# Performance work log

Measured on AMD Instinct MI355X. Metric: run time of the kernel, lower is better.

Reference implementation:

```python
import jax, jax.numpy as jnp
import numpy as np

N_NODES = 50000
N_EDGES = 800000
N_GRAPHS = 64
HEADS = 8
HID = 16
D = HEADS * HID  # 128
N_CLASSES = 10
NEG_SLOPE = 0.2
N_LAYERS = 5


def setup_inputs() -> dict:
    key = jax.random.key(0)
    ks = jax.random.split(key, 12)
    x = jax.random.normal(ks[0], (N_NODES, D), dtype=jnp.float32)
    edge_index = jax.random.randint(ks[1], (2, N_EDGES), 0, N_NODES, dtype=jnp.int32)
    batch = jnp.sort(jax.random.randint(ks[2], (N_NODES,), 0, N_GRAPHS, dtype=jnp.int32))
    s = 1.0 / np.sqrt(D)
    # all 5 GATv2 layers share the same shapes (in = 8*hidden = 128); stack on axis 0
    Wl = jax.random.normal(ks[3], (N_LAYERS, D, D), dtype=jnp.float32) * s
    bl = jnp.zeros((N_LAYERS, D), dtype=jnp.float32)
    Wr = jax.random.normal(ks[4], (N_LAYERS, D, D), dtype=jnp.float32) * s
    br = jnp.zeros((N_LAYERS, D), dtype=jnp.float32)
    att = jax.random.normal(ks[5], (N_LAYERS, HEADS, HID), dtype=jnp.float32) * (1.0 / np.sqrt(HID))
    bias = jnp.zeros((N_LAYERS, D), dtype=jnp.float32)
    Wout = jax.random.normal(ks[6], (D, N_CLASSES), dtype=jnp.float32) * s
    bout = jnp.zeros((N_CLASSES,), dtype=jnp.float32)
    return {"x": x, "edge_index": edge_index, "batch": batch,
            "Wl": Wl, "bl": bl, "Wr": Wr, "br": br, "att": att, "bias": bias,
            "Wout": Wout, "bout": bout}


def gatv2_layer(x, src, dst, Wl, bl, Wr, br, att, bias):
    # x: [N, D_in]; returns [N, HEADS*HID]
    n = x.shape[0]
    xl = (x @ Wl + bl).reshape(n, HEADS, HID)   # source/message transform
    xr = (x @ Wr + br).reshape(n, HEADS, HID)   # target transform
    # GATv2 attention: att . leaky_relu(xl_j + xr_i) per edge, per head
    e = jax.nn.leaky_relu(xl[src] + xr[dst], NEG_SLOPE)          # [E, H, C]
    logits = jnp.einsum('ehc,hc->eh', e, att)                    # [E, H]
    # segment-softmax over incoming edges of each dst node
    m = jax.ops.segment_max(logits, dst, num_segments=n)         # [N, H]
    p = jnp.exp(logits - m[dst])
    denom = jax.ops.segment_sum(p, dst, num_segments=n)          # [N, H]
    alpha = p / denom[dst]                                       # [E, H]
    msg = xl[src] * alpha[:, :, None]                            # [E, H, C]
    out = jax.ops.segment_sum(msg, dst, num_segments=n)
    return out.reshape(n, HEADS * HID) + bias


def reference(x, edge_index, batch, Wl, bl, Wr, br, att, bias, Wout, bout):
    n = x.shape[0]
    # GATv2Conv(add_self_loops=True): append self loops to the edge list
    loops = jnp.arange(n, dtype=edge_index.dtype)
    src = jnp.concatenate([edge_index[0], loops])
    dst = jnp.concatenate([edge_index[1], loops])
    h = x
    for l in range(N_LAYERS):
        h = gatv2_layer(h, src, dst, Wl[l], bl[l], Wr[l], br[l], att[l], bias[l])
        h = jax.nn.elu(h)
    # global mean pool over graphs
    sums = jax.ops.segment_sum(h, batch, num_segments=N_GRAPHS)       # [G, D]
    counts = jax.ops.segment_sum(jnp.ones((n,), h.dtype), batch, num_segments=N_GRAPHS)
    pooled = sums / jnp.maximum(counts, 1.0)[:, None]
    logits = pooled @ Wout + bout
    return jax.nn.log_softmax(logits, axis=1)
```

## Files before the change

kernel.cpp:

```cpp
#include <hip/hip_runtime.h>
#include <hip/hip_bf16.h>
#include <math.h>

#define DD 128
#define HEADS 8
#define HID 16
#define NEG_SLOPE 0.2f
#define N_LAYERS 5
#define N_GRAPHS 64
#define N_CLASSES 10

typedef __bf16 bf16x8 __attribute__((ext_vector_type(8)));
typedef float f32x4 __attribute__((ext_vector_type(4)));

__device__ __forceinline__ float bflo(unsigned u) { return __uint_as_float(u << 16); }
__device__ __forceinline__ float bfhi(unsigned u) { return __uint_as_float(u & 0xffff0000u); }
__device__ __forceinline__ float bf1(unsigned short us) { return __uint_as_float(((unsigned)us) << 16); }
__device__ __forceinline__ unsigned short f2bf(float f) {
    unsigned u = __float_as_uint(f);
    u += 0x7fffu + ((u >> 16) & 1u);
    return (unsigned short)(u >> 16);
}
__device__ __forceinline__ unsigned pack2bf(float a, float b) {
    return (unsigned)f2bf(a) | ((unsigned)f2bf(b) << 16);
}

#define WCNT (N_LAYERS * 4 * 16 * 64)


__global__ void k_setup(const float* __restrict__ x, unsigned* __restrict__ xb,
                        const float* __restrict__ Wl, const float* __restrict__ Wr,
                        unsigned short* __restrict__ wB, int* __restrict__ deg,
                        float* __restrict__ pooled, float* __restrict__ counts,
                        int n2, int n_nodes) {
    int id = blockIdx.x * 256 + threadIdx.x;
    if (id < n2) {
        float2 v = *(const float2*)(x + 2 * (size_t)id);
        xb[id] = pack2bf(v.x, v.y);
        return;
    }
    id -= n2;
    if (id < WCNT) {
        int lane = id & 63;
        int ntg  = (id >> 6) & 15;
        int ks   = (id >> 10) & 3;
        int l    = id >> 12;
        int q = lane >> 4, r = lane & 15;
        int n = ntg * 16 + r;
        const float* W = ((n < DD) ? Wl : Wr) + (size_t)l * DD * DD;
        int nn = n & (DD - 1);
        size_t off = (size_t)l * (4 * 16 * 64 * 8) + ((size_t)(ks * 16 + ntg) * 64 + lane) * 8;
        for (int j = 0; j < 8; ++j) {
            int k = ks * 32 + q * 8 + j;
            wB[off + j] = f2bf(W[(size_t)k * DD + nn]);
        }
        return;
    }
    id -= WCNT;
    if (id < n_nodes) { deg[id] = 0; return; }
    id -= n_nodes;
    if (id < N_GRAPHS * DD) { pooled[id] = 0.f; return; }
    id -= N_GRAPHS * DD;
    if (id < N_GRAPHS) counts[id] = 0.f;
}


__global__ void k_deg_count(const int* __restrict__ ei, int* __restrict__ deg,
                            int n_edges, int n_total) {
    int e = blockIdx.x * 256 + threadIdx.x;
    if (e >= n_total) return;
    int d = (e < n_edges) ? ei[n_edges + e] : (e - n_edges);
    atomicAdd(&deg[d], 1);
}

__global__ void k_scan_blk(const int* __restrict__ deg, int* __restrict__ tmp,
                           int* __restrict__ btot, int n) {
    __shared__ int wsum[4];
    int tid = threadIdx.x, wv = tid >> 6, ln = tid & 63;
    int i = blockIdx.x * 256 + tid;
    int v = (i < n) ? deg[i] : 0;
    int x = v;
#pragma unroll
    for (int ofs = 1; ofs < 64; ofs <<= 1) {
        int t = __shfl_up(x, ofs);
        if (ln >= ofs) x += t;
    }
    if (ln == 63) wsum[wv] = x;
    __syncthreads();
    int off = 0;
    for (int k = 0; k < wv; k++) off += wsum[k];
    int incl = off + x;
    if (i < n) tmp[i] = incl;
    if (tid == 255) btot[blockIdx.x] = incl;
}

__global__ void k_scan_tot(int* __restrict__ btot, int nb) {
    __shared__ int wsum[4];
    int tid = threadIdx.x, wv = tid >> 6, ln = tid & 63;
    int v = (tid < nb) ? btot[tid] : 0;
    int x = v;
#pragma unroll
    for (int ofs = 1; ofs < 64; ofs <<= 1) {
        int t = __shfl_up(x, ofs);
        if (ln >= ofs) x += t;
    }
    if (ln == 63) wsum[wv] = x;
    __syncthreads();
    int off = 0;
    for (int k = 0; k < wv; k++) off += wsum[k];
    if (tid < nb) btot[tid] = off + x;
}

__global__ void k_scan_fix(const int* __restrict__ deg, const int* __restrict__ tmp,
                           const int* __restrict__ btot, int* __restrict__ row_ptr,
                           int* __restrict__ cursor, int n) {
    int b = blockIdx.x;
    int i = b * 256 + threadIdx.x;
    if (i >= n) return;
    int base = (b > 0) ? btot[b - 1] : 0;
    int incl = base + tmp[i];
    row_ptr[i + 1] = incl;
    cursor[i] = incl - deg[i];
    if (i == 0) row_ptr[0] = 0;
}

__global__ void k_scatter(const int* __restrict__ ei, int* __restrict__ cursor,
                          int* __restrict__ csr_src, int n_edges, int n_total) {
    int e = blockIdx.x * 256 + threadIdx.x;
    if (e >= n_total) return;
    int s, d;
    if (e < n_edges) { s = ei[e]; d = ei[n_edges + e]; }
    else { s = d = e - n_edges; }
    int pos = atomicAdd(&cursor[d], 1);
    csr_src[pos] = s;
}


__global__ __launch_bounds__(256) void k_gemm_mfma(
    const unsigned short* __restrict__ in, const unsigned short* __restrict__ wB,
    const float* __restrict__ bl, const float* __restrict__ br,
    unsigned short* __restrict__ xl, unsigned short* __restrict__ xr, int n_nodes) {
    int w = threadIdx.x >> 6;
    int lane = threadIdx.x & 63;
    int q = lane >> 4, r = lane & 15;
    int blk = blockIdx.x;

    f32x4 acc[4][4] = {};
#pragma unroll
    for (int ks = 0; ks < 4; ++ks) {
        bf16x8 bh[4];
#pragma unroll
        for (int nt = 0; nt < 4; ++nt) {
            int ntg = w * 4 + nt;
            bh[nt] = *(const bf16x8*)(wB + ((size_t)(ks * 16 + ntg) * 64 + lane) * 8);
        }
        bf16x8 ah[4];
#pragma unroll
        for (int mt = 0; mt < 4; ++mt) {
            int node = blk * 64 + mt * 16 + r;
            if (node >= n_nodes) node = n_nodes - 1;
            ah[mt] = *(const bf16x8*)(in + (size_t)node * DD + ks * 32 + q * 8);
        }
#pragma unroll
        for (int mt = 0; mt < 4; ++mt)
#pragma unroll
            for (int nt = 0; nt < 4; ++nt)
                acc[mt][nt] = __builtin_amdgcn_mfma_f32_16x16x32_bf16(ah[mt], bh[nt], acc[mt][nt], 0, 0, 0);
    }
#pragma unroll
    for (int nt = 0; nt < 4; ++nt) {
        int col = w * 64 + nt * 16 + r;
        float bv = (col < DD) ? bl[col] : br[col - DD];
        unsigned short* dstbase = (col < DD) ? (xl + col) : (xr + (col - DD));
#pragma unroll
        for (int mt = 0; mt < 4; ++mt)
#pragma unroll
            for (int reg = 0; reg < 4; ++reg) {
                int node = blk * 64 + mt * 16 + q * 4 + reg;
                if (node < n_nodes)
                    dstbase[(size_t)node * DD] = f2bf(acc[mt][nt][reg] + bv);
            }
    }
}


__global__ __launch_bounds__(256) void k_node_agg(
    const unsigned short* __restrict__ xl, const unsigned short* __restrict__ xr,
    const int* __restrict__ row_ptr, const int* __restrict__ csr_src,
    const float* __restrict__ att, const float* __restrict__ bias,
    unsigned short* __restrict__ h_out, int n_nodes) {
    int wave = threadIdx.x >> 6;
    int lane = threadIdx.x & 63;
    int node = blockIdx.x * 4 + wave;
    if (node >= n_nodes) return;
    int grp = lane >> 4, sl = lane & 15;
    int beg = row_ptr[node], end = row_ptr[node + 1];

    uint4 xru = *(const uint4*)(xr + (size_t)node * DD + sl * 8);
    float xr0 = bflo(xru.x), xr1 = bfhi(xru.x), xr2 = bflo(xru.y), xr3 = bfhi(xru.y);
    float xr4 = bflo(xru.z), xr5 = bfhi(xru.z), xr6 = bflo(xru.w), xr7 = bfhi(xru.w);
    float4 at0 = *(const float4*)(att + sl * 8);
    float4 at1 = *(const float4*)(att + sl * 8 + 4);

    float l = 0.f;
    float a0 = 0.f, a1 = 0.f, a2 = 0.f, a3 = 0.f, a4 = 0.f, a5 = 0.f, a6 = 0.f, a7 = 0.f;

    int t0 = beg + grp;
    uint4 xu = make_uint4(0u, 0u, 0u, 0u);
    int sidx = 0;
    if (t0 < end) {
        int s = csr_src[t0];
        xu = *(const uint4*)(xl + (size_t)s * DD + sl * 8);
    }
    if (t0 + 4 < end) sidx = csr_src[t0 + 4];

    for (int t = t0; t < end; t += 4) {
        uint4 cur = xu;
        int snew = 0;
        if (t + 8 < end) snew = csr_src[t + 8];
        if (t + 4 < end) xu = *(const uint4*)(xl + (size_t)sidx * DD + sl * 8);
        sidx = snew;

        float x0 = bflo(cur.x), x1 = bfhi(cur.x), x2 = bflo(cur.y), x3 = bfhi(cur.y);
        float x4 = bflo(cur.z), x5 = bfhi(cur.z), x6 = bflo(cur.w), x7 = bfhi(cur.w);
        float v0 = x0 + xr0; v0 = v0 > 0.f ? v0 : NEG_SLOPE * v0;
        float v1 = x1 + xr1; v1 = v1 > 0.f ? v1 : NEG_SLOPE * v1;
        float v2 = x2 + xr2; v2 = v2 > 0.f ? v2 : NEG_SLOPE * v2;
        float v3 = x3 + xr3; v3 = v3 > 0.f ? v3 : NEG_SLOPE * v3;
        float v4 = x4 + xr4; v4 = v4 > 0.f ? v4 : NEG_SLOPE * v4;
        float v5 = x5 + xr5; v5 = v5 > 0.f ? v5 : NEG_SLOPE * v5;
        float v6 = x6 + xr6; v6 = v6 > 0.f ? v6 : NEG_SLOPE * v6;
        float v7 = x7 + xr7; v7 = v7 > 0.f ? v7 : NEG_SLOPE * v7;
        float lg = at0.x * v0 + at0.y * v1 + at0.z * v2 + at0.w * v3 +
                   at1.x * v4 + at1.y * v5 + at1.z * v6 + at1.w * v7;
        lg += __shfl_xor(lg, 1);
        float p = __expf(lg);
        l += p;
        a0 += p * x0; a1 += p * x1; a2 += p * x2; a3 += p * x3;
        a4 += p * x4; a5 += p * x5; a6 += p * x6; a7 += p * x7;
    }
    l  += __shfl_xor(l, 16);  l  += __shfl_xor(l, 32);
    a0 += __shfl_xor(a0, 16); a0 += __shfl_xor(a0, 32);
    a1 += __shfl_xor(a1, 16); a1 += __shfl_xor(a1, 32);
    a2 += __shfl_xor(a2, 16); a2 += __shfl_xor(a2, 32);
    a3 += __shfl_xor(a3, 16); a3 += __shfl_xor(a3, 32);
    a4 += __shfl_xor(a4, 16); a4 += __shfl_xor(a4, 32);
    a5 += __shfl_xor(a5, 16); a5 += __shfl_xor(a5, 32);
    a6 += __shfl_xor(a6, 16); a6 += __shfl_xor(a6, 32);
    a7 += __shfl_xor(a7, 16); a7 += __shfl_xor(a7, 32);

    if (grp == 0) {
        float4 bv0 = *(const float4*)(bias + sl * 8);
        float4 bv1 = *(const float4*)(bias + sl * 8 + 4);
        float rl = 1.f / l;
        float o0 = a0 * rl + bv0.x; o0 = o0 > 0.f ? o0 : __expf(o0) - 1.f;
        float o1 = a1 * rl + bv0.y; o1 = o1 > 0.f ? o1 : __expf(o1) - 1.f;
        float o2 = a2 * rl + bv0.z; o2 = o2 > 0.f ? o2 : __expf(o2) - 1.f;
        float o3 = a3 * rl + bv0.w; o3 = o3 > 0.f ? o3 : __expf(o3) - 1.f;
        float o4 = a4 * rl + bv1.x; o4 = o4 > 0.f ? o4 : __expf(o4) - 1.f;
        float o5 = a5 * rl + bv1.y; o5 = o5 > 0.f ? o5 : __expf(o5) - 1.f;
        float o6 = a6 * rl + bv1.z; o6 = o6 > 0.f ? o6 : __expf(o6) - 1.f;
        float o7 = a7 * rl + bv1.w; o7 = o7 > 0.f ? o7 : __expf(o7) - 1.f;
        uint4 o;
        o.x = pack2bf(o0, o1); o.y = pack2bf(o2, o3);
        o.z = pack2bf(o4, o5); o.w = pack2bf(o6, o7);
        *(uint4*)(h_out + (size_t)node * DD + sl * 8) = o;
    }
}


__global__ void k_pool2(const unsigned short* __restrict__ h, const int* __restrict__ batch,
                        float* __restrict__ pooled, float* __restrict__ counts,
                        int n_nodes, int chunk) {
    int c = threadIdx.x;
    int beg = blockIdx.x * chunk;
    if (beg >= n_nodes) return;
    int end = beg + chunk; if (end > n_nodes) end = n_nodes;
    int cur = batch[beg];
    float acc = 0.f; int cnt = 0;
    for (int node = beg; node < end; ++node) {
        int g = batch[node];
        if (g != cur) {
            atomicAdd(&pooled[cur * DD + c], acc);
            if (c == 0) atomicAdd(&counts[cur], (float)cnt);
            acc = 0.f; cnt = 0; cur = g;
        }
        acc += bf1(h[(size_t)node * DD + c]);
        cnt++;
    }
    atomicAdd(&pooled[cur * DD + c], acc);
    if (c == 0) atomicAdd(&counts[cur], (float)cnt);
}

__global__ void k_final(const float* __restrict__ pooled, const float* __restrict__ counts,
                        const float* __restrict__ Wout, const float* __restrict__ bout,
                        float* __restrict__ out) {
    __shared__ float slog[N_GRAPHS * N_CLASSES];
    int t = threadIdx.x;
    int g = t / N_CLASSES, c = t % N_CLASSES;
    float cnt = fmaxf(counts[g], 1.f);
    float acc = bout[c];
    for (int k = 0; k < DD; k++)
        acc += (pooled[g * DD + k] / cnt) * Wout[k * N_CLASSES + c];
    slog[t] = acc;
    __syncthreads();
    float mx = -INFINITY;
    for (int j = 0; j < N_CLASSES; j++) mx = fmaxf(mx, slog[g * N_CLASSES + j]);
    float se = 0.f;
    for (int j = 0; j < N_CLASSES; j++) se += __expf(slog[g * N_CLASSES + j] - mx);
    out[t] = acc - mx - __logf(se);
}

extern "C" void kernel_launch(void* const* d_in, const int* in_sizes, int n_in,
                              void* d_out, int out_size, void* d_ws, size_t ws_size,
                              hipStream_t stream) {
    const float* x     = (const float*)d_in[0];
    const int*   ei    = (const int*)d_in[1];
    const int*   batch = (const int*)d_in[2];
    const float* Wl    = (const float*)d_in[3];
    const float* bl    = (const float*)d_in[4];
    const float* Wr    = (const float*)d_in[5];
    const float* br    = (const float*)d_in[6];
    const float* att   = (const float*)d_in[7];
    const float* bias  = (const float*)d_in[8];
    const float* Wout  = (const float*)d_in[9];
    const float* bout  = (const float*)d_in[10];
    float* out = (float*)d_out;

    int n_nodes = in_sizes[0] / DD;
    int n_edges = in_sizes[1] / 2;
    int n_total = n_edges + n_nodes;
    int ND = n_nodes * DD;

    const int WPL = 4 * 16 * 64 * 8;

    unsigned short* hb  = (unsigned short*)d_ws;
    unsigned short* xb  = hb + (size_t)ND;
    unsigned short* xlb = xb + (size_t)ND;
    unsigned short* xrb = xlb + (size_t)ND;
    unsigned short* wB  = xrb + (size_t)ND;
    int*    deg         = (int*)(wB + (size_t)N_LAYERS * WPL);
    int*    row_ptr     = deg + n_nodes;
    int*    cursor      = row_ptr + (n_nodes + 1);
    int*    csr_src     = cursor + n_nodes;
    int*    scan_tmp    = csr_src + n_total;
    int*    btot        = scan_tmp + n_nodes;
    float*  pooled      = (float*)(btot + 256);
    float*  counts      = pooled + N_GRAPHS * DD;

    dim3 b256(256);
    int gE    = (n_total + 255) / 256;
    int gNode = (n_nodes + 255) / 256;
    int gGemm = (n_nodes + 63) / 64;
    int gAgg  = (n_nodes + 3) / 4;
    int poolBlocks = 1024;
    int poolChunk = (n_nodes + poolBlocks - 1) / poolBlocks;

    int n2 = ND / 2;
    int setupTotal = n2 + WCNT + n_nodes + N_GRAPHS * DD + N_GRAPHS;
    k_setup<<<(setupTotal + 255) / 256, b256, 0, stream>>>(x, (unsigned*)xb, Wl, Wr, wB,
                                                           deg, pooled, counts, n2, n_nodes);
    k_deg_count<<<gE, b256, 0, stream>>>(ei, deg, n_edges, n_total);
    k_scan_blk<<<gNode, b256, 0, stream>>>(deg, scan_tmp, btot, n_nodes);
    k_scan_tot<<<1, b256, 0, stream>>>(btot, gNode);
    k_scan_fix<<<gNode, b256, 0, stream>>>(deg, scan_tmp, btot, row_ptr, cursor, n_nodes);
    k_scatter<<<gE, b256, 0, stream>>>(ei, cursor, csr_src, n_edges, n_total);

    for (int l = 0; l < N_LAYERS; l++) {
        const float* bl_l   = bl   + (size_t)l * DD;
        const float* br_l   = br   + (size_t)l * DD;
        const float* att_l  = att  + (size_t)l * HEADS * HID;
        const float* bias_l = bias + (size_t)l * DD;
        const unsigned short* in = (l == 0) ? xb : hb;

        k_gemm_mfma<<<gGemm, b256, 0, stream>>>(in, wB + (size_t)l * WPL, bl_l, br_l,
                                                xlb, xrb, n_nodes);
        k_node_agg<<<gAgg, b256, 0, stream>>>(xlb, xrb, row_ptr, csr_src, att_l, bias_l, hb, n_nodes);
    }

    k_pool2<<<poolBlocks, dim3(128), 0, stream>>>(hb, batch, pooled, counts, n_nodes, poolChunk);
    k_final<<<1, dim3(N_GRAPHS * N_CLASSES), 0, stream>>>(pooled, counts, Wout, bout, out);
}
```

Before: 566.1 us.

## Build CSR via two-level binned counting sort with shared-memory atomics

Replaces the global-atomic degree count, three-pass node scan and global-atomic scatter with a bucketed counting sort. Edges are first histogrammed into 256 destination bins per block, scanned, and scattered into bins as packed (src,dst) 16-bit pairs. Each bin is then sorted locally in LDS to produce row_ptr and csr_src. This removes heavy contended global atomics and random global writes, but it assumes node ids fit in 16 bits and that each bin holds at most 8192 edges and 256 nodes.

```diff
diff --git a/kernel.cpp b/kernel.cpp
--- a/kernel.cpp
+++ b/kernel.cpp
@@ -9,6 +9,8 @@
 #define N_LAYERS 5
 #define N_GRAPHS 64
 #define N_CLASSES 10
+#define NBINS 256
+#define BIN_CAP 8192
 
 typedef __bf16 bf16x8 __attribute__((ext_vector_type(8)));
 typedef float f32x4 __attribute__((ext_vector_type(4)));
@@ -30,9 +32,8 @@
 
 __global__ void k_setup(const float* __restrict__ x, unsigned* __restrict__ xb,
                         const float* __restrict__ Wl, const float* __restrict__ Wr,
-                        unsigned short* __restrict__ wB, int* __restrict__ deg,
-                        float* __restrict__ pooled, float* __restrict__ counts,
-                        int n2, int n_nodes) {
+                        unsigned short* __restrict__ wB,
+                        float* __restrict__ pooled, float* __restrict__ counts, int n2) {
     int id = blockIdx.x * 256 + threadIdx.x;
     if (id < n2) {
         float2 v = *(const float2*)(x + 2 * (size_t)id);
@@ -57,82 +58,131 @@
         return;
     }
     id -= WCNT;
-    if (id < n_nodes) { deg[id] = 0; return; }
-    id -= n_nodes;
     if (id < N_GRAPHS * DD) { pooled[id] = 0.f; return; }
     id -= N_GRAPHS * DD;
     if (id < N_GRAPHS) counts[id] = 0.f;
 }
 
 
-__global__ void k_deg_count(const int* __restrict__ ei, int* __restrict__ deg,
-                            int n_edges, int n_total) {
-    int e = blockIdx.x * 256 + threadIdx.x;
-    if (e >= n_total) return;
-    int d = (e < n_edges) ? ei[n_edges + e] : (e - n_edges);
-    atomicAdd(&deg[d], 1);
-}
-
-__global__ void k_scan_blk(const int* __restrict__ deg, int* __restrict__ tmp,
-                           int* __restrict__ btot, int n) {
+__global__ __launch_bounds__(256) void k_bin_cnt(const int* __restrict__ ei,
+        int* __restrict__ cnt, int n_edges, int n_total, int chunk,
+        unsigned long long bin_mul) {
+    __shared__ int hist[NBINS];
+    int tid = threadIdx.x;
+    hist[tid] = 0;
+    __syncthreads();
+    int beg = blockIdx.x * chunk;
+    int end = beg + chunk; if (end > n_total) end = n_total;
+    for (int e = beg + tid; e < end; e += 256) {
+        int d = (e < n_edges) ? ei[n_edges + e] : (e - n_edges);
+        int b = (int)(((unsigned long long)(unsigned)d * bin_mul) >> 32);
+        atomicAdd(&hist[b], 1);
+    }
+    __syncthreads();
+    cnt[tid * 256 + blockIdx.x] = hist[tid];
+}
+
+__global__ __launch_bounds__(256) void k_bin_scan(int* __restrict__ cnt, int* __restrict__ btot) {
     __shared__ int wsum[4];
-    int tid = threadIdx.x, wv = tid >> 6, ln = tid & 63;
-    int i = blockIdx.x * 256 + tid;
-    int v = (i < n) ? deg[i] : 0;
+    int b = blockIdx.x, t = threadIdx.x, wv = t >> 6, ln = t & 63;
+    int v = cnt[b * 256 + t];
     int x = v;
 #pragma unroll
     for (int ofs = 1; ofs < 64; ofs <<= 1) {
-        int t = __shfl_up(x, ofs);
-        if (ln >= ofs) x += t;
+        int tt = __shfl_up(x, ofs);
+        if (ln >= ofs) x += tt;
     }
     if (ln == 63) wsum[wv] = x;
     __syncthreads();
     int off = 0;
     for (int k = 0; k < wv; k++) off += wsum[k];
     int incl = off + x;
-    if (i < n) tmp[i] = incl;
-    if (tid == 255) btot[blockIdx.x] = incl;
-}
-
-__global__ void k_scan_tot(int* __restrict__ btot, int nb) {
+    cnt[b * 256 + t] = incl - v;
+    if (t == 255) btot[b] = incl;
+}
+
+__global__ __launch_bounds__(256) void k_tot_scan(const int* __restrict__ btot,
+        int* __restrict__ bin_start, int* __restrict__ row_ptr, int n_nodes) {
     __shared__ int wsum[4];
-    int tid = threadIdx.x, wv = tid >> 6, ln = tid & 63;
-    int v = (tid < nb) ? btot[tid] : 0;
+    int t = threadIdx.x, wv = t >> 6, ln = t & 63;
+    int v = btot[t];
     int x = v;
 #pragma unroll
     for (int ofs = 1; ofs < 64; ofs <<= 1) {
-        int t = __shfl_up(x, ofs);
-        if (ln >= ofs) x += t;
+        int tt = __shfl_up(x, ofs);
+        if (ln >= ofs) x += tt;
     }
     if (ln == 63) wsum[wv] = x;
     __syncthreads();
     int off = 0;
     for (int k = 0; k < wv; k++) off += wsum[k];
-    if (tid < nb) btot[tid] = off + x;
-}
-
-__global__ void k_scan_fix(const int* __restrict__ deg, const int* __restrict__ tmp,
-                           const int* __restrict__ btot, int* __restrict__ row_ptr,
-                           int* __restrict__ cursor, int n) {
-    int b = blockIdx.x;
-    int i = b * 256 + threadIdx.x;
-    if (i >= n) return;
-    int base = (b > 0) ? btot[b - 1] : 0;
-    int incl = base + tmp[i];
-    row_ptr[i + 1] = incl;
-    cursor[i] = incl - deg[i];
-    if (i == 0) row_ptr[0] = 0;
-}
-
-__global__ void k_scatter(const int* __restrict__ ei, int* __restrict__ cursor,
-                          int* __restrict__ csr_src, int n_edges, int n_total) {
-    int e = blockIdx.x * 256 + threadIdx.x;
-    if (e >= n_total) return;
-    int s, d;
-    if (e < n_edges) { s = ei[e]; d = ei[n_edges + e]; }
-    else { s = d = e - n_edges; }
-    int pos = atomicAdd(&cursor[d], 1);
-    csr_src[pos] = s;
+    int incl = off + x;
+    bin_start[t] = incl - v;
+    if (t == 255) { bin_start[256] = incl; row_ptr[n_nodes] = incl; }
+}
+
+__global__ __launch_bounds__(256) void k_bin_scatter(const int* __restrict__ ei,
+        const int* __restrict__ cnt, const int* __restrict__ bin_start,
+        unsigned* __restrict__ binned, int n_edges, int n_total, int chunk,
+        unsigned long long bin_mul) {
+    __shared__ int cur[NBINS];
+    int tid = threadIdx.x;
+    cur[tid] = bin_start[tid] + cnt[tid * 256 + blockIdx.x];
+    __syncthreads();
+    int beg = blockIdx.x * chunk;
+    int end = beg + chunk; if (end > n_total) end = n_total;
+    for (int e = beg + tid; e < end; e += 256) {
+        int s, d;
+        if (e < n_edges) { s = ei[e]; d = ei[n_edges + e]; }
+        else { s = d = e - n_edges; }
+        int b = (int)(((unsigned long long)(unsigned)d * bin_mul) >> 32);
+        int pos = atomicAdd(&cur[b], 1);
+        binned[pos] = (unsigned)s | ((unsigned)d << 16);
+    }
+}
+
+__global__ __launch_bounds__(256) void k_bin_csr(const unsigned* __restrict__ binned,
+        const int* __restrict__ bin_start, int* __restrict__ csr_src,
+        int* __restrict__ row_ptr, int n_nodes, unsigned long long bin_mul) {
+    __shared__ int sbuf[BIN_CAP];
+    __shared__ int ldeg[256];
+    __shared__ int wsum[4];
+    int b = blockIdx.x, t = threadIdx.x, wv = t >> 6, ln = t & 63;
+    int lo = (int)(((((unsigned long long)b) << 32) + bin_mul - 1) / bin_mul);
+    int hi = (int)(((((unsigned long long)(b + 1)) << 32) + bin_mul - 1) / bin_mul);
+    if (hi > n_nodes) hi = n_nodes;
+    int estart = bin_start[b], eend = bin_start[b + 1];
+    int ne = eend - estart;
+    ldeg[t] = 0;
+    __syncthreads();
+    for (int k = t; k < ne; k += 256) {
+        unsigned v = binned[estart + k];
+        atomicAdd(&ldeg[(int)(v >> 16) - lo], 1);
+    }
+    __syncthreads();
+    int vdeg = ldeg[t];
+    int x = vdeg;
+#pragma unroll
+    for (int ofs = 1; ofs < 64; ofs <<= 1) {
+        int tt = __shfl_up(x, ofs);
+        if (ln >= ofs) x += tt;
+    }
+    if (ln == 63) wsum[wv] = x;
+    __syncthreads();
+    int off = 0;
+    for (int k = 0; k < wv; k++) off += wsum[k];
+    int excl = off + x - vdeg;
+    if (lo + t < hi) row_ptr[lo + t] = estart + excl;
+    ldeg[t] = excl;
+    __syncthreads();
+    for (int k = t; k < ne; k += 256) {
+        unsigned v = binned[estart + k];
+        int pos = atomicAdd(&ldeg[(int)(v >> 16) - lo], 1);
+        sbuf[pos] = (int)(v & 0xffffu);
+    }
+    __syncthreads();
+    for (int k = t; k < ne; k += 256)
+        csr_src[estart + k] = sbuf[k];
 }
 
 
@@ -333,38 +383,39 @@
     int ND = n_nodes * DD;
 
     const int WPL = 4 * 16 * 64 * 8;
+    unsigned long long bin_mul = (((unsigned long long)NBINS) << 32) / (unsigned)n_nodes;
 
     unsigned short* hb  = (unsigned short*)d_ws;
     unsigned short* xb  = hb + (size_t)ND;
     unsigned short* xlb = xb + (size_t)ND;
     unsigned short* xrb = xlb + (size_t)ND;
     unsigned short* wB  = xrb + (size_t)ND;
-    int*    deg         = (int*)(wB + (size_t)N_LAYERS * WPL);
-    int*    row_ptr     = deg + n_nodes;
-    int*    cursor      = row_ptr + (n_nodes + 1);
-    int*    csr_src     = cursor + n_nodes;
-    int*    scan_tmp    = csr_src + n_total;
-    int*    btot        = scan_tmp + n_nodes;
-    float*  pooled      = (float*)(btot + 256);
-    float*  counts      = pooled + N_GRAPHS * DD;
+    int*      cnt       = (int*)(wB + (size_t)N_LAYERS * WPL);
+    int*      btot      = cnt + NBINS * 256;
+    int*      bin_start = btot + NBINS;
+    unsigned* binned    = (unsigned*)(bin_start + NBINS + 1);
+    int*      csr_src   = (int*)(binned + n_total);
+    int*      row_ptr   = csr_src + n_total;
+    float*    pooled    = (float*)(row_ptr + n_nodes + 1);
+    float*    counts    = pooled + N_GRAPHS * DD;
 
     dim3 b256(256);
-    int gE    = (n_total + 255) / 256;
-    int gNode = (n_nodes + 255) / 256;
     int gGemm = (n_nodes + 63) / 64;
     int gAgg  = (n_nodes + 3) / 4;
+    int chunk = (n_total + 255) / 256;
     int poolBlocks = 1024;
     int poolChunk = (n_nodes + poolBlocks - 1) / poolBlocks;
 
     int n2 = ND / 2;
-    int setupTotal = n2 + WCNT + n_nodes + N_GRAPHS * DD + N_GRAPHS;
+    int setupTotal = n2 + WCNT + N_GRAPHS * DD + N_GRAPHS;
     k_setup<<<(setupTotal + 255) / 256, b256, 0, stream>>>(x, (unsigned*)xb, Wl, Wr, wB,
-                                                           deg, pooled, counts, n2, n_nodes);
-    k_deg_count<<<gE, b256, 0, stream>>>(ei, deg, n_edges, n_total);
-    k_scan_blk<<<gNode, b256, 0, stream>>>(deg, scan_tmp, btot, n_nodes);
-    k_scan_tot<<<1, b256, 0, stream>>>(btot, gNode);
-    k_scan_fix<<<gNode, b256, 0, stream>>>(deg, scan_tmp, btot, row_ptr, cursor, n_nodes);
-    k_scatter<<<gE, b256, 0, stream>>>(ei, cursor, csr_src, n_edges, n_total);
+                                                           pooled, counts, n2);
+    k_bin_cnt<<<256, b256, 0, stream>>>(ei, cnt, n_edges, n_total, chunk, bin_mul);
+    k_bin_scan<<<NBINS, b256, 0, stream>>>(cnt, btot);
+    k_tot_scan<<<1, b256, 0, stream>>>(btot, bin_start, row_ptr, n_nodes);
+    k_bin_scatter<<<256, b256, 0, stream>>>(ei, cnt, bin_start, binned, n_edges, n_total,
+                                            chunk, bin_mul);
+    k_bin_csr<<<NBINS, b256, 0, stream>>>(binned, bin_start, csr_src, row_ptr, n_nodes, bin_mul);
 
     for (int l = 0; l < N_LAYERS; l++) {
         const float* bl_l   = bl   + (size_t)l * DD;
```

After: 498.3 us. -12.0%, faster.
